# Optimization experiments

Measured on AMD Instinct MI355X. Metric: run time of the kernel, lower is better.

## Reference

```python
import jax, jax.numpy as jnp
import numpy as np


def setup_inputs() -> dict:
    key = jax.random.key(0)
    ks = jax.random.split(key, 9)
    B, D_IN, UNITS, TOPICS, VOCAB = 64, 512, 1024, 20, 32000
    return {
        "inputs": jax.random.normal(ks[0], (B, D_IN), jnp.float32),
        "prev_state": jax.random.normal(ks[1], (B, UNITS), jnp.float32),
        "kernel": jax.random.normal(ks[2], (D_IN, UNITS), jnp.float32) * 0.02,
        "recurrent_kernel": jax.random.normal(ks[3], (UNITS, UNITS), jnp.float32) * 0.02,
        "bernoli_kernel": jax.random.normal(ks[4], (UNITS, 1), jnp.float32) * 0.02,
        "vocab_kernel": jax.random.normal(ks[5], (UNITS, VOCAB), jnp.float32) * 0.02,
        "beta": jax.random.normal(ks[6], (TOPICS, VOCAB), jnp.float32),
        "indicators": jax.random.randint(ks[7], (B,), 0, 2, jnp.int32),
        "indices": jax.random.randint(ks[8], (B,), 0, VOCAB, jnp.int32),
    }


def reference(inputs, prev_state, kernel, recurrent_kernel, bernoli_kernel,
              vocab_kernel, beta, indicators, indices):
    # h_t = x @ W_xh + h_{t-1} @ W_hh   -> [B, units]
    next_state = inputs @ kernel + prev_state @ recurrent_kernel
    # stop-word Bernoulli prob: sigmoid(softplus(h_t @ w_b))  -> [B, 1]
    bern_p = jax.nn.sigmoid(jax.nn.softplus(next_state @ bernoli_kernel))
    bern_p = bern_p[..., None]  # [B, 1, 1]
    # deterministic sampling key (reference baseline)
    samp_key = jax.random.key(42)
    bern_samples = jax.random.bernoulli(samp_key, bern_p).astype(jnp.float32)
    # logits: [B,1,V] + (1 - l_t) * beta[T,V] -> [B, T, V]
    logits = (next_state @ vocab_kernel)[:, None, :] + (1.0 - bern_samples) * beta
    word_prob_out = jax.nn.softmax(logits, axis=-1)
    return word_prob_out, next_state
```

## Files before the change

### kernel.cpp

```cpp
#include <hip/hip_runtime.h>
#include <cstdint>
#include <cstddef>

typedef unsigned int u32;
typedef unsigned short u16;

#define NB 64
#define DIN 512
#define UNITS 1024
#define TOPICS 20
#define VOCAB 32000
#define NS_OFF ((size_t)NB * TOPICS * VOCAB)

typedef __attribute__((ext_vector_type(8))) short s16x8;
typedef __attribute__((ext_vector_type(4))) float f32x4;

__device__ __forceinline__ float bf2f(u16 h) {
    union { u32 u; float f; } c; c.u = ((u32)h) << 16; return c.f;
}
__device__ __forceinline__ u16 f2bf(float f) {
    union { float f; u32 u; } c; c.f = f;
    u32 r = c.u + 0x7FFFu + ((c.u >> 16) & 1u);
    return (u16)(r >> 16);
}
template<bool F32>
__device__ __forceinline__ float ldv(const void* p, size_t i) {
    if constexpr (F32) return ((const float*)p)[i];
    else return bf2f(((const u16*)p)[i]);
}
__device__ __forceinline__ float ldr(const void* p, size_t i, bool f32) {
    return f32 ? ((const float*)p)[i] : bf2f(((const u16*)p)[i]);
}

__device__ __forceinline__ u32 threefry_bits_partitionable(u32 i) {
    const u32 ks0 = 0u, ks1 = 42u, ks2 = 0u ^ 42u ^ 0x1BD11BDAu;
    u32 x0 = 0u + ks0, x1 = i + ks1;
#define TF_R(r) { x0 += x1; x1 = (x1 << r) | (x1 >> (32 - r)); x1 ^= x0; }
    TF_R(13) TF_R(15) TF_R(26) TF_R(6)
    x0 += ks1; x1 += ks2 + 1u;
    TF_R(17) TF_R(29) TF_R(16) TF_R(24)
    x0 += ks2; x1 += ks0 + 2u;
    TF_R(13) TF_R(15) TF_R(26) TF_R(6)
    x0 += ks0; x1 += ks1 + 3u;
    TF_R(17) TF_R(29) TF_R(16) TF_R(24)
    x0 += ks1; x1 += ks2 + 4u;
    TF_R(13) TF_R(15) TF_R(26) TF_R(6)
    x0 += ks2; x1 += ks0 + 5u;
#undef TF_R
    return x0 ^ x1;
}

__global__ __launch_bounds__(256)
void k_init(const void* __restrict__ beta, int* __restrict__ flag,
            float* __restrict__ lsum, float* __restrict__ eb) {
    int tid = threadIdx.x, lane = tid & 63, w = tid >> 6;
    __shared__ int cnt_s[4];
    int cnt = 0;
    const u32* braw = (const u32*)beta;
    for (int i = tid; i < 1024; i += 256) {
        u32 x = braw[i];
        u32 e = (x >> 7) & 0xFFu;
        cnt += (e >= 110u && e <= 132u) ? 1 : 0;
    }
    for (int off = 32; off; off >>= 1) cnt += __shfl_down(cnt, off, 64);
    if (lane == 0) cnt_s[w] = cnt;
    __syncthreads();
    int total = cnt_s[0] + cnt_s[1] + cnt_s[2] + cnt_s[3];
    bool f32 = total < 512;

    size_t base = (size_t)blockIdx.x * 2000;
    for (int i = tid; i < 2000; i += 256)
        eb[base + i] = __expf(ldr(beta, base + i, f32));

    if (blockIdx.x == 0) {
        for (int i = tid; i < NB * TOPICS; i += 256) lsum[i] = 0.f;
        if (tid == 0) flag[0] = f32 ? 1 : 0;
    }
}

template<bool F32>
__device__ void state_body(const void* xin, const void* h0, const void* Wxh,
                           const void* Whh, float* ns_f32, void* dout) {
    __shared__ float lx[DIN + UNITS];
    int b = blockIdx.x >> 2;
    int u = ((blockIdx.x & 3) << 8) | threadIdx.x;
    for (int i = threadIdx.x; i < DIN; i += 256)
        lx[i] = ldv<F32>(xin, (size_t)b * DIN + i);
    for (int i = threadIdx.x; i < UNITS; i += 256)
        lx[DIN + i] = ldv<F32>(h0, (size_t)b * UNITS + i);
    __syncthreads();
    float acc = 0.f;
#pragma unroll 8
    for (int k = 0; k < DIN; ++k)   acc += lx[k]       * ldv<F32>(Wxh, (size_t)k * UNITS + u);
#pragma unroll 8
    for (int k = 0; k < UNITS; ++k) acc += lx[DIN + k] * ldv<F32>(Whh, (size_t)k * UNITS + u);
    int idx = b * UNITS + u;
    ns_f32[idx] = acc;
    if constexpr (F32) ((float*)dout)[NS_OFF + idx] = acc;
    else               ((u16*)dout)[NS_OFF + idx]   = f2bf(acc);
}
__global__ __launch_bounds__(256)
void k_state(const int* __restrict__ flag, const void* xin, const void* h0,
             const void* Wxh, const void* Whh,
             float* __restrict__ ns_f32, void* dout) {
    if (*flag) state_body<true>(xin, h0, Wxh, Whh, ns_f32, dout);
    else       state_body<false>(xin, h0, Wxh, Whh, ns_f32, dout);
}

template<bool F32>
__device__ void bern_body(const float* ns, const void* bk, float* coeff) {
    int b = blockIdx.x, lane = threadIdx.x;
    float s = 0.f;
#pragma unroll
    for (int i = 0; i < UNITS / 64; ++i) {
        int k = lane + (i << 6);
        s += ns[b * UNITS + k] * ldv<F32>(bk, k);
    }
    for (int off = 32; off; off >>= 1) s += __shfl_down(s, off, 64);
    if (lane == 0) {
        float sp = log1pf(expf(s));
        float p  = 1.f / (1.f + expf(-sp));
        u32 bits = threefry_bits_partitionable((u32)b);
        union { u32 u; float f; } c; c.u = (bits >> 9) | 0x3f800000u;
        float uni = c.f - 1.0f;
        coeff[b] = (uni < p) ? 0.f : 1.f;
    }
}
__global__ __launch_bounds__(64)
void k_bern(const int* __restrict__ flag, const float* __restrict__ ns,
            const void* bk, float* __restrict__ coeff) {
    if (*flag) bern_body<true>(ns, bk, coeff);
    else       bern_body<false>(ns, bk, coeff);
}

#define PAD 68
#define SV_SMEM_BYTES (2 * 64 * PAD * 4)

__device__ __forceinline__ void sv_mfma_body(const short* __restrict__ ns16,
                                             const short* __restrict__ Wv,
                                             float* __restrict__ esv,
                                             char* smem_raw) {
    short* As = (short*)smem_raw;
    const int tid  = threadIdx.x;
    const int lane = tid & 63;
    const int wn   = tid >> 6;
    const int v0   = blockIdx.x * 64;
    const int col  = v0 + wn * 16 + (lane & 15);
    const int krow = (lane >> 4) * 8;

    const short* Bcol = Wv + col;

    f32x4 acc[4];
#pragma unroll
    for (int m = 0; m < 4; ++m) acc[m] = (f32x4){0.f, 0.f, 0.f, 0.f};

    short bA[16], bB[16];

    auto loadB = [&](short* buf, int t) {
#pragma unroll
        for (int kf = 0; kf < 2; ++kf)
#pragma unroll
            for (int e = 0; e < 8; ++e)
                buf[kf * 8 + e] = Bcol[(size_t)(t * 64 + kf * 32 + krow + e) * VOCAB];
    };
    auto stageA = [&](int dbase, int t) {
#pragma unroll
        for (int r = 0; r < 2; ++r) {
            int e = tid + r * 256;
            int row = e >> 3, c = e & 7;
            s16x8 v = *(const s16x8*)&ns16[(size_t)row * UNITS + t * 64 + c * 8];
            *(s16x8*)&As[dbase + row * 64 + ((c * 8) ^ ((row & 7) << 3))] = v;
        }
    };
    auto compute = [&](int dbase, const short* buf) {
        s16x8 aF[4][2];
#pragma unroll
        for (int mf = 0; mf < 4; ++mf)
#pragma unroll
            for (int kf = 0; kf < 2; ++kf) {
                int row = mf * 16 + (lane & 15);
                int co  = (kf * 32 + krow) ^ ((row & 7) << 3);
                aF[mf][kf] = *(const s16x8*)&As[dbase + row * 64 + co];
            }
#pragma unroll
        for (int kf = 0; kf < 2; ++kf) {
            s16x8 bF;
#pragma unroll
            for (int e = 0; e < 8; ++e) bF[e] = buf[kf * 8 + e];
#pragma unroll
            for (int mf = 0; mf < 4; ++mf)
                acc[mf] = __builtin_amdgcn_mfma_f32_16x16x32_bf16(
                              aF[mf][kf], bF, acc[mf], 0, 0, 0);
        }
    };

    loadB(bA, 0);
    for (int t = 0; t < 16; t += 2) {
        stageA(0, t);
        __syncthreads();
        loadB(bB, t + 1);
        compute(0, bA);
        stageA(64 * 64, t + 1);
        __syncthreads();
        if (t + 2 < 16) loadB(bA, t + 2);
        compute(64 * 64, bB);
    }

#pragma unroll
    for (int mf = 0; mf < 4; ++mf)
#pragma unroll
        for (int r = 0; r < 4; ++r) {
            int b = mf * 16 + (lane >> 4) * 4 + r;
            esv[(size_t)b * VOCAB + col] = __expf(acc[mf][r]);
        }
}

__device__ void sv_f32_body(const float* __restrict__ ns, const float* __restrict__ Wv,
                            float* __restrict__ esv, float* As, float* Bs) {
    int tid = threadIdx.x;
    int vt = tid & 7;
    int bg = tid >> 3;
    int v0 = blockIdx.x * 64;
    float acc[2][8];
#pragma unroll
    for (int r = 0; r < 2; ++r)
#pragma unroll
        for (int j = 0; j < 8; ++j) acc[r][j] = 0.f;

    for (int k0 = 0; k0 < UNITS; k0 += 64) {
        __syncthreads();
        for (int e = tid; e < 1024; e += 256) {
            int row = e >> 4, c4 = e & 15;
            *(float4*)&As[row * PAD + c4 * 4] =
                *(const float4*)&ns[row * UNITS + k0 + c4 * 4];
        }
        for (int e = tid; e < 1024; e += 256) {
            int row = e >> 4, c4 = e & 15;
            *(float4*)&Bs[row * PAD + c4 * 4] =
                *(const float4*)(Wv + (size_t)(k0 + row) * VOCAB + v0 + c4 * 4);
        }
        __syncthreads();
#pragma unroll 4
        for (int u = 0; u < 64; u += 4) {
            float4 a0 = *(float4*)&As[(bg * 2 + 0) * PAD + u];
            float4 a1 = *(float4*)&As[(bg * 2 + 1) * PAD + u];
            float aa0[4] = {a0.x, a0.y, a0.z, a0.w};
            float aa1[4] = {a1.x, a1.y, a1.z, a1.w};
#pragma unroll
            for (int uu = 0; uu < 4; ++uu) {
                float4 b0 = *(float4*)&Bs[(u + uu) * PAD + vt * 8];
                float4 b1 = *(float4*)&Bs[(u + uu) * PAD + vt * 8 + 4];
                float bb[8] = {b0.x, b0.y, b0.z, b0.w, b1.x, b1.y, b1.z, b1.w};
#pragma unroll
                for (int j = 0; j < 8; ++j) {
                    acc[0][j] = fmaf(aa0[uu], bb[j], acc[0][j]);
                    acc[1][j] = fmaf(aa1[uu], bb[j], acc[1][j]);
                }
            }
        }
    }
#pragma unroll
    for (int r = 0; r < 2; ++r) {
        float4 e0, e1;
        e0.x = __expf(acc[r][0]); e0.y = __expf(acc[r][1]);
        e0.z = __expf(acc[r][2]); e0.w = __expf(acc[r][3]);
        e1.x = __expf(acc[r][4]); e1.y = __expf(acc[r][5]);
        e1.z = __expf(acc[r][6]); e1.w = __expf(acc[r][7]);
        float* dst = esv + (size_t)(bg * 2 + r) * VOCAB + v0 + vt * 8;
        *(float4*)dst = e0;
        *(float4*)(dst + 4) = e1;
    }
}

__global__ __launch_bounds__(256)
void k_sv(const int* __restrict__ flag, const float* __restrict__ ns,
          const void* Wv, const void* dout, float* __restrict__ esv) {
    __shared__ __align__(16) char smem[SV_SMEM_BYTES];
    if (*flag) {
        float* As = (float*)smem;
        sv_f32_body(ns, (const float*)Wv, esv, As, As + 64 * PAD);
    } else {
        sv_mfma_body((const short*)dout + NS_OFF, (const short*)Wv, esv, smem);
    }
}

__global__ __launch_bounds__(256)
void k_sum(const float* __restrict__ esv, const float* __restrict__ eb,
           const float* __restrict__ coeff, float* __restrict__ lsum) {
    int b = blockIdx.y, tid = threadIdx.x;
    float c = coeff[b];
    const float4* e4 = (const float4*)(esv + (size_t)b * VOCAB);
    int i0 = blockIdx.x * 256 + tid;
    __shared__ float red[4][TOPICS];
    int lane = tid & 63, w = tid >> 6;

    if (c != 0.f) {
        float acc[TOPICS];
#pragma unroll
        for (int t = 0; t < TOPICS; ++t) acc[t] = 0.f;
        for (int i = i0; i < VOCAB / 4; i += 4096) {
            float4 e = e4[i];
#pragma unroll
            for (int t = 0; t < TOPICS; ++t) {
                float4 g = *(const float4*)(eb + (size_t)t * VOCAB + i * 4);
                acc[t] += e.x * g.x + e.y * g.y + e.z * g.z + e.w * g.w;
            }
        }
#pragma unroll
        for (int t = 0; t < TOPICS; ++t) {
            float v = acc[t];
            for (int off = 32; off; off >>= 1) v += __shfl_down(v, off, 64);
            if (lane == 0) red[w][t] = v;
        }
        __syncthreads();
        if (tid < TOPICS) {
            float s = red[0][tid] + red[1][tid] + red[2][tid] + red[3][tid];
            atomicAdd(&lsum[b * TOPICS + tid], s);
        }
    } else {
        float a = 0.f;
        for (int i = i0; i < VOCAB / 4; i += 4096) {
            float4 e = e4[i];
            a += e.x + e.y + e.z + e.w;
        }
        for (int off = 32; off; off >>= 1) a += __shfl_down(a, off, 64);
        if (lane == 0) red[w][0] = a;
        __syncthreads();
        if (tid < TOPICS) {
            float s = red[0][0] + red[1][0] + red[2][0] + red[3][0];
            atomicAdd(&lsum[b * TOPICS + tid], s);
        }
    }
}

template<bool F32>
__device__ void write_body(const float* esv, const float* eb, const float* coeff,
                           const float* lsum, void* dout) {
    int b = blockIdx.y, tid = threadIdx.x;
    int v0 = blockIdx.x * 2048 + tid * 8;
    if (v0 >= VOCAB) return;
    float c = coeff[b];
    const float* er = esv + (size_t)b * VOCAB + v0;
    float4 e0 = *(const float4*)er;
    float4 e1 = *(const float4*)(er + 4);
#pragma unroll 4
    for (int t = 0; t < TOPICS; ++t) {
        float inv = 1.0f / lsum[b * TOPICS + t];
        float o0, o1, o2, o3, o4, o5, o6, o7;
        if (c != 0.f) {
            const float* gr = eb + (size_t)t * VOCAB + v0;
            float4 g0 = *(const float4*)gr;
            float4 g1 = *(const float4*)(gr + 4);
            o0 = e0.x * g0.x * inv; o1 = e0.y * g0.y * inv;
            o2 = e0.z * g0.z * inv; o3 = e0.w * g0.w * inv;
            o4 = e1.x * g1.x * inv; o5 = e1.y * g1.y * inv;
            o6 = e1.z * g1.z * inv; o7 = e1.w * g1.w * inv;
        } else {
            o0 = e0.x * inv; o1 = e0.y * inv; o2 = e0.z * inv; o3 = e0.w * inv;
            o4 = e1.x * inv; o5 = e1.y * inv; o6 = e1.z * inv; o7 = e1.w * inv;
        }
        size_t off = (size_t)b * TOPICS * VOCAB + (size_t)t * VOCAB + v0;
        if constexpr (F32) {
            float4 s0 = {o0, o1, o2, o3}, s1 = {o4, o5, o6, o7};
            *(float4*)((float*)dout + off) = s0;
            *(float4*)((float*)dout + off + 4) = s1;
        } else {
            uint4 st;
            st.x = (u32)f2bf(o0) | ((u32)f2bf(o1) << 16);
            st.y = (u32)f2bf(o2) | ((u32)f2bf(o3) << 16);
            st.z = (u32)f2bf(o4) | ((u32)f2bf(o5) << 16);
            st.w = (u32)f2bf(o6) | ((u32)f2bf(o7) << 16);
            *(uint4*)((u16*)dout + off) = st;
        }
    }
}
__global__ __launch_bounds__(256)
void k_write(const int* __restrict__ flag, const float* __restrict__ esv,
             const float* __restrict__ eb, const float* __restrict__ coeff,
             const float* __restrict__ lsum, void* dout) {
    if (*flag) write_body<true>(esv, eb, coeff, lsum, dout);
    else       write_body<false>(esv, eb, coeff, lsum, dout);
}

extern "C" void kernel_launch(void* const* d_in, const int* in_sizes, int n_in,
                              void* d_out, int out_size, void* d_ws, size_t ws_size,
                              hipStream_t stream) {
    const void* xin  = d_in[0];
    const void* h0   = d_in[1];
    const void* Wxh  = d_in[2];
    const void* Whh  = d_in[3];
    const void* bk   = d_in[4];
    const void* Wv   = d_in[5];
    const void* beta = d_in[6];

    char* ws = (char*)d_ws;
    int*   flag   = (int*)  (ws + 0);
    float* coeff  = (float*)(ws + 256);
    float* lsum   = (float*)(ws + 1024);
    float* ns_f32 = (float*)(ws + 8192);
    float* eb     = (float*)(ws + 270336);
    float* esv    = (float*)(ws + 2830336);

    k_init <<<320, 256, 0, stream>>>(beta, flag, lsum, eb);
    k_state<<<256, 256, 0, stream>>>(flag, xin, h0, Wxh, Whh, ns_f32, d_out);
    k_bern <<<64, 64, 0, stream>>>(flag, ns_f32, bk, coeff);
    k_sv   <<<500, 256, 0, stream>>>(flag, ns_f32, Wv, d_out, esv);
    k_sum  <<<dim3(16, 64), 256, 0, stream>>>(esv, eb, coeff, lsum);
    k_write<<<dim3(16, 64), 256, 0, stream>>>(flag, esv, eb, coeff, lsum, d_out);
}
```

Before: 482.6 us.

## Stage vocab GEMM tiles via direct global-to-LDS loads with 4-deep pipeline

Replaces the per-lane strided global loads of the vocab kernel (B operand) and the register-staged A tile with global_load_lds transfers of both A and B tiles into a 4-buffer shared-memory ring. Three stages are prefetched ahead, and explicit vmcnt waits plus barriers sequence each k-step. The aim is to remove uncoalesced column-strided B reads and register round trips while hiding load latency. The cost is more LDS per block (64KB), which may lower occupancy, and fragile hand-counted vmcnt values.

```diff
diff --git a/kernel.cpp b/kernel.cpp
--- a/kernel.cpp
+++ b/kernel.cpp
@@ -134,78 +134,84 @@
 }
 
 #define PAD 68
-#define SV_SMEM_BYTES (2 * 64 * PAD * 4)
-
-__device__ __forceinline__ void sv_mfma_body(const short* __restrict__ ns16,
-                                             const short* __restrict__ Wv,
-                                             float* __restrict__ esv,
-                                             char* smem_raw) {
-    short* As = (short*)smem_raw;
+#define SV_STAGE_B 16384
+#define SV_SMEM_BYTES (4 * SV_STAGE_B)
+
+__device__ __forceinline__ void gld16(const void* g, void* l) {
+    __builtin_amdgcn_global_load_lds(
+        (const __attribute__((address_space(1))) void*)g,
+        (__attribute__((address_space(3))) void*)l, 16, 0, 0);
+}
+
+__device__ __forceinline__ void sv_stage(const short* __restrict__ ns16,
+                                         const short* __restrict__ Wv,
+                                         char* smem, int buf, int t, int v0,
+                                         int wn, int lane) {
+    char* sb = smem + buf * SV_STAGE_B;
+#pragma unroll
+    for (int r = 0; r < 2; ++r) {
+        int ib = r * 256 + wn * 64;
+        int i  = ib + lane;
+        const short* gA = ns16 + (size_t)(i >> 3) * UNITS + t * 64
+                        + (((i & 7) ^ ((i >> 3) & 7)) << 3);
+        gld16(gA, sb + (size_t)ib * 16);
+        const short* gB = Wv + (size_t)(t * 64 + (i >> 3)) * VOCAB + v0 + ((i & 7) << 3);
+        gld16(gB, sb + 8192 + (size_t)ib * 16);
+    }
+}
+
+__device__ __forceinline__ void sv_compute(const char* smem, int buf,
+                                           int lane, int wn, f32x4 acc[4]) {
+    const char*  sb = smem + buf * SV_STAGE_B;
+    const short* Bs = (const short*)(sb + 8192);
+#pragma unroll
+    for (int kk = 0; kk < 2; ++kk) {
+        s16x8 bf;
+#pragma unroll
+        for (int e = 0; e < 8; ++e)
+            bf[e] = Bs[(kk * 32 + ((lane >> 4) << 3) + e) * 64 + wn * 16 + (lane & 15)];
+#pragma unroll
+        for (int mf = 0; mf < 4; ++mf) {
+            int row  = mf * 16 + (lane & 15);
+            int slot = (kk * 4 + (lane >> 4)) ^ (row & 7);
+            s16x8 af = *(const s16x8*)(sb + row * 128 + slot * 16);
+            acc[mf] = __builtin_amdgcn_mfma_f32_16x16x32_bf16(af, bf, acc[mf], 0, 0, 0);
+        }
+    }
+}
+
+__device__ void sv_mfma_body(const short* __restrict__ ns16,
+                             const short* __restrict__ Wv,
+                             float* __restrict__ esv, char* smem) {
     const int tid  = threadIdx.x;
     const int lane = tid & 63;
     const int wn   = tid >> 6;
     const int v0   = blockIdx.x * 64;
-    const int col  = v0 + wn * 16 + (lane & 15);
-    const int krow = (lane >> 4) * 8;
-
-    const short* Bcol = Wv + col;
 
     f32x4 acc[4];
 #pragma unroll
     for (int m = 0; m < 4; ++m) acc[m] = (f32x4){0.f, 0.f, 0.f, 0.f};
 
-    short bA[16], bB[16];
-
-    auto loadB = [&](short* buf, int t) {
-#pragma unroll
-        for (int kf = 0; kf < 2; ++kf)
-#pragma unroll
-            for (int e = 0; e < 8; ++e)
-                buf[kf * 8 + e] = Bcol[(size_t)(t * 64 + kf * 32 + krow + e) * VOCAB];
-    };
-    auto stageA = [&](int dbase, int t) {
-#pragma unroll
-        for (int r = 0; r < 2; ++r) {
-            int e = tid + r * 256;
-            int row = e >> 3, c = e & 7;
-            s16x8 v = *(const s16x8*)&ns16[(size_t)row * UNITS + t * 64 + c * 8];
-            *(s16x8*)&As[dbase + row * 64 + ((c * 8) ^ ((row & 7) << 3))] = v;
-        }
-    };
-    auto compute = [&](int dbase, const short* buf) {
-        s16x8 aF[4][2];
-#pragma unroll
-        for (int mf = 0; mf < 4; ++mf)
-#pragma unroll
-            for (int kf = 0; kf < 2; ++kf) {
-                int row = mf * 16 + (lane & 15);
-                int co  = (kf * 32 + krow) ^ ((row & 7) << 3);
-                aF[mf][kf] = *(const s16x8*)&As[dbase + row * 64 + co];
-            }
-#pragma unroll
-        for (int kf = 0; kf < 2; ++kf) {
-            s16x8 bF;
-#pragma unroll
-            for (int e = 0; e < 8; ++e) bF[e] = buf[kf * 8 + e];
-#pragma unroll
-            for (int mf = 0; mf < 4; ++mf)
-                acc[mf] = __builtin_amdgcn_mfma_f32_16x16x32_bf16(
-                              aF[mf][kf], bF, acc[mf], 0, 0, 0);
-        }
-    };
-
-    loadB(bA, 0);
-    for (int t = 0; t < 16; t += 2) {
-        stageA(0, t);
-        __syncthreads();
-        loadB(bB, t + 1);
-        compute(0, bA);
-        stageA(64 * 64, t + 1);
-        __syncthreads();
-        if (t + 2 < 16) loadB(bA, t + 2);
-        compute(64 * 64, bB);
-    }
-
+    sv_stage(ns16, Wv, smem, 0, 0, v0, wn, lane);
+    sv_stage(ns16, Wv, smem, 1, 1, v0, wn, lane);
+    sv_stage(ns16, Wv, smem, 2, 2, v0, wn, lane);
+
+#define SV_STEP(T, VM)                                                        \
+    asm volatile("s_waitcnt vmcnt(" #VM ")" ::: "memory");                    \
+    __builtin_amdgcn_s_barrier();                                             \
+    sv_compute(smem, (T) & 3, lane, wn, acc);                                 \
+    __builtin_amdgcn_s_barrier();                                             \
+    asm volatile("" ::: "memory");                                            \
+    if ((T) + 3 < 16)                                                         \
+        sv_stage(ns16, Wv, smem, ((T) + 3) & 3, (T) + 3, v0, wn, lane);
+
+    SV_STEP(0, 8)  SV_STEP(1, 8)  SV_STEP(2, 8)  SV_STEP(3, 8)
+    SV_STEP(4, 8)  SV_STEP(5, 8)  SV_STEP(6, 8)  SV_STEP(7, 8)
+    SV_STEP(8, 8)  SV_STEP(9, 8)  SV_STEP(10, 8) SV_STEP(11, 8)
+    SV_STEP(12, 8) SV_STEP(13, 8) SV_STEP(14, 4) SV_STEP(15, 0)
+#undef SV_STEP
+
+    const int col = v0 + wn * 16 + (lane & 15);
 #pragma unroll
     for (int mf = 0; mf < 4; ++mf)
 #pragma unroll
```

After: 472.2 us. 1.02x faster.

## Split-K vocab GEMM with LDS-staged B tiles and XCD-aware block mapping

Applied to the files above, without the earlier changes.

The bf16 vocab projection now uses 256-wide vocab tiles split into four K-chunks. B tiles are loaded into swizzled LDS with double buffering through global_load_lds, and the A chunk stays resident in LDS. Each block writes raw partial logits to one of four slabs, and the exp moves into k_sum and k_write, which add the partials first. This replaces the uncoalesced strided per-lane B loads with better reuse, at the cost of extra global traffic for the partial slabs and an exp computed in both downstream kernels. Blocks are also remapped by XCD so that neighbouring tiles share L2.

```diff
diff --git a/kernel.cpp b/kernel.cpp
--- a/kernel.cpp
+++ b/kernel.cpp
@@ -11,6 +11,7 @@
 #define TOPICS 20
 #define VOCAB 32000
 #define NS_OFF ((size_t)NB * TOPICS * VOCAB)
+#define ESV_PART ((size_t)NB * VOCAB)
 
 typedef __attribute__((ext_vector_type(8))) short s16x8;
 typedef __attribute__((ext_vector_type(4))) float f32x4;
@@ -134,93 +135,108 @@
 }
 
 #define PAD 68
-#define SV_SMEM_BYTES (2 * 64 * PAD * 4)
-
-__device__ __forceinline__ void sv_mfma_body(const short* __restrict__ ns16,
-                                             const short* __restrict__ Wv,
-                                             float* __restrict__ esv,
-                                             char* smem_raw) {
-    short* As = (short*)smem_raw;
+#define SV_A_STRIDE 264
+#define SV_A_BYTES  (64 * SV_A_STRIDE * 2)
+#define SV_B_BYTES  16384
+#define SV_SMEM_BYTES (SV_A_BYTES + 2 * SV_B_BYTES)
+
+__device__ __forceinline__ void gld16(const void* g, void* l) {
+    __builtin_amdgcn_global_load_lds(
+        (const __attribute__((address_space(1))) void*)g,
+        (__attribute__((address_space(3))) void*)l, 16, 0, 0);
+}
+
+__device__ void sv_mfma_body(const short* __restrict__ ns16,
+                             const short* __restrict__ Wv,
+                             float* __restrict__ esv4, char* smem, int pos) {
+    short* As = (short*)smem;
+    char*  B0 = smem + SV_A_BYTES;
     const int tid  = threadIdx.x;
     const int lane = tid & 63;
     const int wn   = tid >> 6;
-    const int v0   = blockIdx.x * 64;
-    const int col  = v0 + wn * 16 + (lane & 15);
-    const int krow = (lane >> 4) * 8;
-
-    const short* Bcol = Wv + col;
-
-    f32x4 acc[4];
-#pragma unroll
-    for (int m = 0; m < 4; ++m) acc[m] = (f32x4){0.f, 0.f, 0.f, 0.f};
-
-    short bA[16], bB[16];
-
-    auto loadB = [&](short* buf, int t) {
-#pragma unroll
-        for (int kf = 0; kf < 2; ++kf)
+    const int g    = lane >> 4;
+    const int l15  = lane & 15;
+
+    const int vb = pos % 125, kb = pos / 125;
+    const int v0 = vb * 256;
+    const int kbase0 = kb * 256;
+
+#pragma unroll
+    for (int j = 0; j < 8; ++j) {
+        int idx = j * 256 + tid;
+        int row = idx >> 5, c = idx & 31;
+        *(s16x8*)&As[row * SV_A_STRIDE + c * 8] =
+            *(const s16x8*)&ns16[(size_t)row * UNITS + kbase0 + c * 8];
+    }
+
+    auto stageB = [&](int t, char* dst) {
+        int kbase = kbase0 + t * 32;
+#pragma unroll
+        for (int p = 0; p < 4; ++p) {
+            int ib = p * 256 + wn * 64;
+            int idx = ib + lane;
+            int k = idx >> 5, c = idx & 31, s = k >> 3;
+            const short* src = Wv + (size_t)(kbase + k) * VOCAB + v0 + ((c ^ s) << 3);
+            gld16(src, dst + (size_t)idx * 16);
+        }
+    };
+
+    f32x4 acc[4][4];
+#pragma unroll
+    for (int m = 0; m < 4; ++m)
+#pragma unroll
+        for (int n = 0; n < 4; ++n) acc[m][n] = (f32x4){0.f, 0.f, 0.f, 0.f};
+
+    stageB(0, B0);
+    __syncthreads();
+
+#pragma unroll
+    for (int t = 0; t < 8; ++t) {
+        char* cur = B0 + (t & 1) * SV_B_BYTES;
+        if (t < 7) stageB(t + 1, B0 + ((t + 1) & 1) * SV_B_BYTES);
+
+        s16x8 af[4];
+#pragma unroll
+        for (int mf = 0; mf < 4; ++mf)
+            af[mf] = *(const s16x8*)&As[(mf * 16 + l15) * SV_A_STRIDE + t * 32 + g * 8];
+
+        const short* Bs = (const short*)cur;
+#pragma unroll
+        for (int nf = 0; nf < 4; ++nf) {
+            int col = wn * 64 + nf * 16 + l15;
+            int b0  = ((col >> 3) ^ g) * 8 + (col & 7);
+            s16x8 bf;
 #pragma unroll
             for (int e = 0; e < 8; ++e)
-                buf[kf * 8 + e] = Bcol[(size_t)(t * 64 + kf * 32 + krow + e) * VOCAB];
-    };
-    auto stageA = [&](int dbase, int t) {
-#pragma unroll
-        for (int r = 0; r < 2; ++r) {
-            int e = tid + r * 256;
-            int row = e >> 3, c = e & 7;
-            s16x8 v = *(const s16x8*)&ns16[(size_t)row * UNITS + t * 64 + c * 8];
-            *(s16x8*)&As[dbase + row * 64 + ((c * 8) ^ ((row & 7) << 3))] = v;
-        }
-    };
-    auto compute = [&](int dbase, const short* buf) {
-        s16x8 aF[4][2];
-#pragma unroll
-        for (int mf = 0; mf < 4; ++mf)
-#pragma unroll
-            for (int kf = 0; kf < 2; ++kf) {
-                int row = mf * 16 + (lane & 15);
-                int co  = (kf * 32 + krow) ^ ((row & 7) << 3);
-                aF[mf][kf] = *(const s16x8*)&As[dbase + row * 64 + co];
+                bf[e] = Bs[(g * 8 + e) * 256 + b0];
+#pragma unroll
+            for (int mf = 0; mf < 4; ++mf)
+                acc[mf][nf] = __builtin_amdgcn_mfma_f32_16x16x32_bf16(
+                                  af[mf], bf, acc[mf][nf], 0, 0, 0);
+        }
+        __syncthreads();
+    }
+
+    float* dst = esv4 + (size_t)kb * ESV_PART + v0;
+#pragma unroll
+    for (int mf = 0; mf < 4; ++mf)
+#pragma unroll
+        for (int nf = 0; nf < 4; ++nf) {
+            int col = wn * 64 + nf * 16 + l15;
+#pragma unroll
+            for (int r = 0; r < 4; ++r) {
+                int b = mf * 16 + (lane >> 4) * 4 + r;
+                dst[(size_t)b * VOCAB + col] = acc[mf][nf][r];
             }
-#pragma unroll
-        for (int kf = 0; kf < 2; ++kf) {
-            s16x8 bF;
-#pragma unroll
-            for (int e = 0; e < 8; ++e) bF[e] = buf[kf * 8 + e];
-#pragma unroll
-            for (int mf = 0; mf < 4; ++mf)
-                acc[mf] = __builtin_amdgcn_mfma_f32_16x16x32_bf16(
-                              aF[mf][kf], bF, acc[mf], 0, 0, 0);
-        }
-    };
-
-    loadB(bA, 0);
-    for (int t = 0; t < 16; t += 2) {
-        stageA(0, t);
-        __syncthreads();
-        loadB(bB, t + 1);
-        compute(0, bA);
-        stageA(64 * 64, t + 1);
-        __syncthreads();
-        if (t + 2 < 16) loadB(bA, t + 2);
-        compute(64 * 64, bB);
-    }
-
-#pragma unroll
-    for (int mf = 0; mf < 4; ++mf)
-#pragma unroll
-        for (int r = 0; r < 4; ++r) {
-            int b = mf * 16 + (lane >> 4) * 4 + r;
-            esv[(size_t)b * VOCAB + col] = __expf(acc[mf][r]);
         }
 }
 
 __device__ void sv_f32_body(const float* __restrict__ ns, const float* __restrict__ Wv,
-                            float* __restrict__ esv, float* As, float* Bs) {
+                            float* __restrict__ esv4, float* As, float* Bs, int pos) {
     int tid = threadIdx.x;
     int vt = tid & 7;
     int bg = tid >> 3;
-    int v0 = blockIdx.x * 64;
+    int v0 = pos * 64;
     float acc[2][8];
 #pragma unroll
     for (int r = 0; r < 2; ++r)
@@ -261,12 +277,9 @@
     }
 #pragma unroll
     for (int r = 0; r < 2; ++r) {
-        float4 e0, e1;
-        e0.x = __expf(acc[r][0]); e0.y = __expf(acc[r][1]);
-        e0.z = __expf(acc[r][2]); e0.w = __expf(acc[r][3]);
-        e1.x = __expf(acc[r][4]); e1.y = __expf(acc[r][5]);
-        e1.z = __expf(acc[r][6]); e1.w = __expf(acc[r][7]);
-        float* dst = esv + (size_t)(bg * 2 + r) * VOCAB + v0 + vt * 8;
+        float4 e0 = {acc[r][0], acc[r][1], acc[r][2], acc[r][3]};
+        float4 e1 = {acc[r][4], acc[r][5], acc[r][6], acc[r][7]};
+        float* dst = esv4 + (size_t)(bg * 2 + r) * VOCAB + v0 + vt * 8;
         *(float4*)dst = e0;
         *(float4*)(dst + 4) = e1;
     }
@@ -274,22 +287,30 @@
 
 __global__ __launch_bounds__(256)
 void k_sv(const int* __restrict__ flag, const float* __restrict__ ns,
-          const void* Wv, const void* dout, float* __restrict__ esv) {
+          const void* Wv, const void* dout, float* __restrict__ esv4) {
     __shared__ __align__(16) char smem[SV_SMEM_BYTES];
+    int lin = blockIdx.x;
+    int xcd = lin & 7, idx = lin >> 3;
+    int pos = (xcd < 4) ? xcd * 63 + idx : 252 + (xcd - 4) * 62 + idx;
     if (*flag) {
         float* As = (float*)smem;
-        sv_f32_body(ns, (const float*)Wv, esv, As, As + 64 * PAD);
+        sv_f32_body(ns, (const float*)Wv, esv4, As, As + 64 * PAD, pos);
     } else {
-        sv_mfma_body((const short*)dout + NS_OFF, (const short*)Wv, esv, smem);
+        sv_mfma_body((const short*)dout + NS_OFF, (const short*)Wv, esv4, smem, pos);
     }
 }
 
 __global__ __launch_bounds__(256)
-void k_sum(const float* __restrict__ esv, const float* __restrict__ eb,
-           const float* __restrict__ coeff, float* __restrict__ lsum) {
+void k_sum(const int* __restrict__ flag, const float* __restrict__ esv4,
+           const float* __restrict__ eb, const float* __restrict__ coeff,
+           float* __restrict__ lsum) {
     int b = blockIdx.y, tid = threadIdx.x;
+    bool f32 = (*flag != 0);
     float c = coeff[b];
-    const float4* e4 = (const float4*)(esv + (size_t)b * VOCAB);
+    const float4* P0 = (const float4*)(esv4 + (size_t)b * VOCAB);
+    const float4* P1 = (const float4*)(esv4 + ESV_PART + (size_t)b * VOCAB);
+    const float4* P2 = (const float4*)(esv4 + 2 * ESV_PART + (size_t)b * VOCAB);
+    const float4* P3 = (const float4*)(esv4 + 3 * ESV_PART + (size_t)b * VOCAB);
     int i0 = blockIdx.x * 256 + tid;
     __shared__ float red[4][TOPICS];
     int lane = tid & 63, w = tid >> 6;
@@ -299,7 +320,15 @@
 #pragma unroll
         for (int t = 0; t < TOPICS; ++t) acc[t] = 0.f;
         for (int i = i0; i < VOCAB / 4; i += 4096) {
-            float4 e = e4[i];
+            float4 q = P0[i];
+            if (!f32) {
+                float4 a = P1[i], d = P2[i], h = P3[i];
+                q.x += a.x + d.x + h.x; q.y += a.y + d.y + h.y;
+                q.z += a.z + d.z + h.z; q.w += a.w + d.w + h.w;
+            }
+            float4 e;
+            e.x = __expf(q.x); e.y = __expf(q.y);
+            e.z = __expf(q.z); e.w = __expf(q.w);
 #pragma unroll
             for (int t = 0; t < TOPICS; ++t) {
                 float4 g = *(const float4*)(eb + (size_t)t * VOCAB + i * 4);
@@ -320,8 +349,13 @@
     } else {
         float a = 0.f;
         for (int i = i0; i < VOCAB / 4; i += 4096) {
-            float4 e = e4[i];
-            a += e.x + e.y + e.z + e.w;
+            float4 q = P0[i];
+            if (!f32) {
+                float4 x = P1[i], d = P2[i], h = P3[i];
+                q.x += x.x + d.x + h.x; q.y += x.y + d.y + h.y;
+                q.z += x.z + d.z + h.z; q.w += x.w + d.w + h.w;
+            }
+            a += __expf(q.x) + __expf(q.y) + __expf(q.z) + __expf(q.w);
         }
         for (int off = 32; off; off >>= 1) a += __shfl_down(a, off, 64);
         if (lane == 0) red[w][0] = a;
@@ -334,15 +368,27 @@
 }
 
 template<bool F32>
-__device__ void write_body(const float* esv, const float* eb, const float* coeff,
+__device__ void write_body(const float* esv4, const float* eb, const float* coeff,
                            const float* lsum, void* dout) {
     int b = blockIdx.y, tid = threadIdx.x;
     int v0 = blockIdx.x * 2048 + tid * 8;
     if (v0 >= VOCAB) return;
     float c = coeff[b];
-    const float* er = esv + (size_t)b * VOCAB + v0;
-    float4 e0 = *(const float4*)er;
-    float4 e1 = *(const float4*)(er + 4);
+    const float* er = esv4 + (size_t)b * VOCAB + v0;
+    float4 q0 = *(const float4*)er;
+    float4 q1 = *(const float4*)(er + 4);
+    if constexpr (!F32) {
+#pragma unroll
+        for (int p = 1; p < 4; ++p) {
+            float4 a0 = *(const float4*)(er + p * ESV_PART);
+            float4 a1 = *(const float4*)(er + p * ESV_PART + 4);
+            q0.x += a0.x; q0.y += a0.y; q0.z += a0.z; q0.w += a0.w;
+            q1.x += a1.x; q1.y += a1.y; q1.z += a1.z; q1.w += a1.w;
+        }
+    }
+    float4 e0, e1;
+    e0.x = __expf(q0.x); e0.y = __expf(q0.y); e0.z = __expf(q0.z); e0.w = __expf(q0.w);
+    e1.x = __expf(q1.x); e1.y = __expf(q1.y); e1.z = __expf(q1.z); e1.w = __expf(q1.w);
 #pragma unroll 4
     for (int t = 0; t < TOPICS; ++t) {
         float inv = 1.0f / lsum[b * TOPICS + t];
@@ -375,11 +421,11 @@
     }
 }
 __global__ __launch_bounds__(256)
-void k_write(const int* __restrict__ flag, const float* __restrict__ esv,
+void k_write(const int* __restrict__ flag, const float* __restrict__ esv4,
              const float* __restrict__ eb, const float* __restrict__ coeff,
              const float* __restrict__ lsum, void* dout) {
-    if (*flag) write_body<true>(esv, eb, coeff, lsum, dout);
-    else       write_body<false>(esv, eb, coeff, lsum, dout);
+    if (*flag) write_body<true>(esv4, eb, coeff, lsum, dout);
+    else       write_body<false>(esv4, eb, coeff, lsum, dout);
 }
 
 extern "C" void kernel_launch(void* const* d_in, const int* in_sizes, int n_in,
@@ -399,12 +445,12 @@
     float* lsum   = (float*)(ws + 1024);
     float* ns_f32 = (float*)(ws + 8192);
     float* eb     = (float*)(ws + 270336);
-    float* esv    = (float*)(ws + 2830336);
+    float* esv4   = (float*)(ws + 2830336);
 
     k_init <<<320, 256, 0, stream>>>(beta, flag, lsum, eb);
     k_state<<<256, 256, 0, stream>>>(flag, xin, h0, Wxh, Whh, ns_f32, d_out);
     k_bern <<<64, 64, 0, stream>>>(flag, ns_f32, bk, coeff);
-    k_sv   <<<500, 256, 0, stream>>>(flag, ns_f32, Wv, d_out, esv);
-    k_sum  <<<dim3(16, 64), 256, 0, stream>>>(esv, eb, coeff, lsum);
-    k_write<<<dim3(16, 64), 256, 0, stream>>>(flag, esv, eb, coeff, lsum, d_out);
-}
+    k_sv   <<<500, 256, 0, stream>>>(flag, ns_f32, Wv, d_out, esv4);
+    k_sum  <<<dim3(16, 64), 256, 0, stream>>>(flag, esv4, eb, coeff, lsum);
+    k_write<<<dim3(16, 64), 256, 0, stream>>>(flag, esv4, eb, coeff, lsum, d_out);
+}
```

New measurement: 551.5 us. +14.3%, slower.
